# Performance work log

Measured on AMD Instinct MI355X. Metric: run time of the kernel, lower is better.

## Reference

```python
import jax, jax.numpy as jnp
import numpy as np

EPS = 1e-12  # F.normalize denominator clamp


def setup_inputs() -> dict:
    key = jax.random.key(0)
    k1, k2, k3, k4 = jax.random.split(key, 4)
    bs, d, nc, ncl, cs, ny = 8192, 768, 64, 500, 100, 1000
    train_embedding = jax.random.normal(k1, (bs, d), dtype=jnp.float32)
    clusters = jax.random.normal(k2, (ncl, cs, d), dtype=jnp.float32)
    # init_concept: uniform in [-0.5, 0.5]
    concept = jax.random.uniform(k3, (d, nc), dtype=jnp.float32, minval=-0.5, maxval=0.5)
    W_h = jax.random.normal(k4, (d, ny), dtype=jnp.float32) * 0.02
    b_h = jnp.zeros((ny,), dtype=jnp.float32)
    return {"train_embedding": train_embedding, "clusters": clusters,
            "concept": concept, "W_h": W_h, "b_h": b_h}


def reference(train_embedding, clusters, concept, W_h, b_h):
    # column-wise L2 normalize concept (F.normalize p=2 dim=0)
    concept_normalized = concept / jnp.maximum(
        jnp.linalg.norm(concept, axis=0, keepdims=True), EPS)
    # projection onto span(concept): C (C^T C)^-1 C^T
    gram = concept.T @ concept                      # [nc, nc]
    proj_matrix = concept @ jnp.linalg.inv(gram) @ concept.T  # [d, d]
    proj = proj_matrix @ train_embedding.T          # [d, bs]
    cluster_mean = jnp.mean(clusters, axis=1)       # [ncl, d]
    score_matrix = jnp.abs(cluster_mean @ concept_normalized)  # [ncl, nc]
    score_norm = score_matrix / jnp.maximum(
        jnp.linalg.norm(score_matrix, axis=0, keepdims=True), EPS)
    L_sparse_1 = jnp.sum(score_norm)
    # sum_{i != j} <score_norm[:,i], score_norm[:,j]> == sum(G) - trace(G)
    G = score_norm.T @ score_norm                   # [nc, nc]
    L_sparse_2 = jnp.sum(G) - jnp.trace(G)
    y_pred = proj.T @ W_h + b_h                     # h_x as linear head, [bs, ny]
    return (y_pred, L_sparse_1, L_sparse_2)
```

## Files before the change

kernel.cpp:

```cpp
#include <hip/hip_runtime.h>
#include <hip/hip_bf16.h>
#include <math.h>

#define BS   8192
#define DD   768
#define NC   64
#define NCL  500
#define CS   100
#define NY   1000
#define EPSN 1e-12f

typedef __attribute__((ext_vector_type(8))) short bf16x8;
typedef __attribute__((ext_vector_type(4))) float f32x4;

union B8 { unsigned u[4]; bf16x8 v; uint4 q; };

__device__ inline unsigned short f2bf(float x) {
    __hip_bfloat16 h = __float2bfloat16(x);
    return *reinterpret_cast<unsigned short*>(&h);
}
__device__ inline unsigned pk2(float a, float b) {
    return (unsigned)f2bf(a) | ((unsigned)f2bf(b) << 16);
}

#define FMA4(acc, s, v) { (acc).x = fmaf((s), (v).x, (acc).x); \
                          (acc).y = fmaf((s), (v).y, (acc).y); \
                          (acc).z = fmaf((s), (v).z, (acc).z); \
                          (acc).w = fmaf((s), (v).w, (acc).w); }

__global__ __launch_bounds__(256) void k_front(
    const float* __restrict__ clusters, const float* __restrict__ C,
    const float* __restrict__ W, const float* __restrict__ X,
    float* __restrict__ cmP, float* __restrict__ gramP,
    float* __restrict__ Up, unsigned short* __restrict__ Tb) {
    __shared__ __align__(16) char smem_raw[25600];
    int b = blockIdx.x, tid = threadIdx.x;
    if (b < 128) {
        uint4 (*CbL)[64] = (uint4(*)[64])smem_raw;
        int r0 = b * 64;
        int w  = tid >> 6, l = tid & 63;
        int rowA = r0 + w*16 + (l & 15);
        int kq   = l >> 4;
        const float* xb = X + (size_t)rowA * DD + kq * 8;
        f32x4 acc[4];
        #pragma unroll
        for (int ng = 0; ng < 4; ++ng) acc[ng] = (f32x4){0.f, 0.f, 0.f, 0.f};
        for (int kc = 0; kc < DD; kc += 64) {
            __syncthreads();
            #pragma unroll
            for (int u = 0; u < 2; ++u) {
                int g = (tid >> 6) + u*4;
                int n = tid & 63;
                const float* cp = C + (size_t)(kc + g*8) * 64 + n;
                uint4 gr;
                gr.x = pk2(cp[0],   cp[64]);
                gr.y = pk2(cp[128], cp[192]);
                gr.z = pk2(cp[256], cp[320]);
                gr.w = pk2(cp[384], cp[448]);
                CbL[g][n] = gr;
            }
            __syncthreads();
            #pragma unroll
            for (int ks2 = 0; ks2 < 2; ++ks2) {
                float4 xa = *((const float4*)(xb + kc + ks2*32));
                float4 xc = *((const float4*)(xb + kc + ks2*32 + 4));
                B8 a;
                a.u[0] = pk2(xa.x, xa.y); a.u[1] = pk2(xa.z, xa.w);
                a.u[2] = pk2(xc.x, xc.y); a.u[3] = pk2(xc.z, xc.w);
                B8 b0, b1, b2, b3;
                b0.q = CbL[ks2*4 + kq][(l & 15)];
                b1.q = CbL[ks2*4 + kq][(l & 15) + 16];
                b2.q = CbL[ks2*4 + kq][(l & 15) + 32];
                b3.q = CbL[ks2*4 + kq][(l & 15) + 48];
                acc[0] = __builtin_amdgcn_mfma_f32_16x16x32_bf16(a.v, b0.v, acc[0], 0, 0, 0);
                acc[1] = __builtin_amdgcn_mfma_f32_16x16x32_bf16(a.v, b1.v, acc[1], 0, 0, 0);
                acc[2] = __builtin_amdgcn_mfma_f32_16x16x32_bf16(a.v, b2.v, acc[2], 0, 0, 0);
                acc[3] = __builtin_amdgcn_mfma_f32_16x16x32_bf16(a.v, b3.v, acc[3], 0, 0, 0);
            }
        }
        int rw = r0 + w*16 + kq * 4;
        #pragma unroll
        for (int ng = 0; ng < 4; ++ng) {
            int n = ng*16 + (l & 15);
            #pragma unroll
            for (int r = 0; r < 4; ++r)
                Tb[(size_t)(rw + r) * 64 + n] = f2bf(acc[ng][r]);
        }
    } else if (b < 1628) {
        int q   = b - 128;
        int sp  = q & 3;
        int idx = (q >> 2) * 256 + tid;
        int r  = idx / 192;
        int d4 = idx % 192;
        const float4* base = (const float4*)clusters
                           + (size_t)r * CS * 192 + (size_t)sp * 25 * 192 + d4;
        float4 a0={0,0,0,0},a1={0,0,0,0},a2={0,0,0,0},a3={0,0,0,0},a4={0,0,0,0};
        for (int s = 0; s < 25; s += 5) {
            float4 v0 = base[(size_t)(s+0)*192];
            float4 v1 = base[(size_t)(s+1)*192];
            float4 v2 = base[(size_t)(s+2)*192];
            float4 v3 = base[(size_t)(s+3)*192];
            float4 v4 = base[(size_t)(s+4)*192];
            a0.x+=v0.x; a0.y+=v0.y; a0.z+=v0.z; a0.w+=v0.w;
            a1.x+=v1.x; a1.y+=v1.y; a1.z+=v1.z; a1.w+=v1.w;
            a2.x+=v2.x; a2.y+=v2.y; a2.z+=v2.z; a2.w+=v2.w;
            a3.x+=v3.x; a3.y+=v3.y; a3.z+=v3.z; a3.w+=v3.w;
            a4.x+=v4.x; a4.y+=v4.y; a4.z+=v4.z; a4.w+=v4.w;
        }
        float4 o;
        o.x = a0.x+a1.x+a2.x+a3.x+a4.x;
        o.y = a0.y+a1.y+a2.y+a3.y+a4.y;
        o.z = a0.z+a1.z+a2.z+a3.z+a4.z;
        o.w = a0.w+a1.w+a2.w+a3.w+a4.w;
        ((float4*)(cmP + (size_t)sp * 384000))[idx] = o;
    } else if (b < 1884) {
        int q  = b - 1628;
        int j  = q & 63, ks = q >> 6;
        int i   = tid & 63;
        int seg = tid >> 6;
        int k0  = ks * 192 + seg * 48;
        float p = 0.f;
        for (int k = k0; k < k0 + 48; ++k)
            p += C[k * NC + i] * C[k * NC + j];
        float (*red)[64] = (float(*)[64])smem_raw;
        red[seg][i] = p;
        __syncthreads();
        if (seg == 0)
            gramP[(size_t)ks * 4096 + i * NC + j] =
                red[0][i] + red[1][i] + red[2][i] + red[3][i];
    } else {
        int q  = b - 1884;
        int nt = q >> 2, ks = q & 3;
        int n0 = nt * 128, kb = ks * 192;
        float (*Cu)[68]  = (float(*)[68])smem_raw;
        float (*Wu)[132] = (float(*)[132])(smem_raw + 8704);
        int tx = tid & 15, ty = tid >> 4;
        float4 a0[4], a1[4];
        #pragma unroll
        for (int i = 0; i < 4; ++i) { a0[i] = make_float4(0,0,0,0); a1[i] = make_float4(0,0,0,0); }
        for (int kc = kb; kc < kb + 192; kc += 32) {
            __syncthreads();
            {   int i4 = tid & 15, kk = tid >> 4;
                *((float4*)&Cu[kk][i4*4])    = *((const float4*)(C + (size_t)(kc+kk)*64 + i4*4));
                *((float4*)&Cu[kk+16][i4*4]) = *((const float4*)(C + (size_t)(kc+kk+16)*64 + i4*4));
            }
            {   int nf = tid & 31, kq2 = tid >> 5;
                #pragma unroll
                for (int u = 0; u < 4; ++u) {
                    int k = kq2 + u * 8;
                    int n = n0 + nf * 4;
                    float4 v = {0.f, 0.f, 0.f, 0.f};
                    if (n < NY) v = *((const float4*)(W + (size_t)(kc + k) * NY + n));
                    *((float4*)&Wu[k][nf*4]) = v;
                }
            }
            __syncthreads();
            #pragma unroll 8
            for (int k = 0; k < 32; ++k) {
                float4 ci = *((float4*)&Cu[k][ty*4]);
                float4 w0 = *((float4*)&Wu[k][tx*8]);
                float4 w1 = *((float4*)&Wu[k][tx*8+4]);
                FMA4(a0[0], ci.x, w0); FMA4(a1[0], ci.x, w1);
                FMA4(a0[1], ci.y, w0); FMA4(a1[1], ci.y, w1);
                FMA4(a0[2], ci.z, w0); FMA4(a1[2], ci.z, w1);
                FMA4(a0[3], ci.w, w0); FMA4(a1[3], ci.w, w1);
            }
        }
        float* Ups = Up + (size_t)ks * 64000;
        #pragma unroll
        for (int i = 0; i < 4; ++i) {
            int irow = ty * 4 + i;
            int n = n0 + tx * 8;
            if (n < NY)     *((float4*)(Ups + (size_t)irow * NY + n))     = a0[i];
            if (n + 4 < NY) *((float4*)(Ups + (size_t)irow * NY + n + 4)) = a1[i];
        }
    }
}

__global__ __launch_bounds__(256) void k_mid(
    const float* __restrict__ gramP, const float* __restrict__ cmP,
    const float* __restrict__ C, float* __restrict__ ginv,
    float* __restrict__ SP) {
    __shared__ __align__(16) char smem_raw[52224];
    int blk = blockIdx.x, tid = threadIdx.x;
    if (blk == 0) {
        int c = tid & 63;
        int q = tid >> 6;
        float a[16], bb[16];
        #pragma unroll
        for (int i = 0; i < 16; ++i) {
            int r = q * 16 + i;
            size_t off = (size_t)r * 64 + c;
            a[i]  = gramP[off] + gramP[4096 + off] + gramP[8192 + off] + gramP[12288 + off];
            bb[i] = (r == c) ? 1.f : 0.f;
        }
        __shared__ float asr[2][64];
        __shared__ float bsr[2][64];
        for (int p = 0; p < 64; ++p) {
            int qp  = p >> 4;
            int lp  = p & 15;
            int par = p & 1;
            if (q == qp) {
                float ap = 0.f, bp = 0.f;
                #pragma unroll
                for (int i = 0; i < 16; ++i)
                    if (i == lp) { ap = a[i]; bp = bb[i]; }
                float App = __shfl(ap, p);
                float s   = 1.0f / App;
                asr[par][c] = ap * s;
                bsr[par][c] = bp * s;
            }
            __syncthreads();
            float as_ = asr[par][c];
            float bs_ = bsr[par][c];
            #pragma unroll
            for (int i = 0; i < 16; ++i) {
                float f = __shfl(a[i], p);
                bool isp = (q == qp) && (i == lp);
                a[i]  = isp ? as_ : fmaf(-f, as_, a[i]);
                bb[i] = isp ? bs_ : fmaf(-f, bs_, bb[i]);
            }
        }
        #pragma unroll
        for (int i = 0; i < 16; ++i)
            ginv[(q * 16 + i) * 64 + c] = bb[i];
    } else {
        int q = blk - 1;
        int tile = q >> 2, ks = q & 3;
        int r0 = tile * 128, kb = ks * 192;
        float (*Mr)[68] = (float(*)[68])smem_raw;
        float (*Cs)[68] = (float(*)[68])(smem_raw + 128*68*4);
        int tx = tid & 15, ty = tid >> 4;
        float4 acc[8];
        #pragma unroll
        for (int r = 0; r < 8; ++r) acc[r] = make_float4(0.f,0.f,0.f,0.f);
        for (int kc = 0; kc < 192; kc += 64) {
            __syncthreads();
            #pragma unroll
            for (int p = 0; p < 8; ++p) {
                int f = tid + p * 256;
                int row = f >> 4, k4 = f & 15;
                int gr = r0 + row;
                int grc = gr < NCL ? gr : (NCL - 1);
                size_t off = (size_t)grc*DD + kb + kc + k4*4;
                float4 c0 = *((const float4*)(cmP + off));
                float4 c1 = *((const float4*)(cmP + 384000 + off));
                float4 c2 = *((const float4*)(cmP + 768000 + off));
                float4 c3 = *((const float4*)(cmP + 1152000 + off));
                float4 m;
                m.x = (c0.x+c1.x+c2.x+c3.x) * 0.01f;
                m.y = (c0.y+c1.y+c2.y+c3.y) * 0.01f;
                m.z = (c0.z+c1.z+c2.z+c3.z) * 0.01f;
                m.w = (c0.w+c1.w+c2.w+c3.w) * 0.01f;
                *((float4*)&Mr[row][k4*4]) = m;
            }
            #pragma unroll
            for (int p = 0; p < 4; ++p) {
                int f = tid + p * 256;
                int k = f >> 4, c4 = f & 15;
                *((float4*)&Cs[k][c4*4]) =
                    *((const float4*)(C + (size_t)(kb+kc+k)*64 + c4*4));
            }
            __syncthreads();
            for (int k0 = 0; k0 < 64; k0 += 4) {
                float4 cv0 = *((float4*)&Cs[k0+0][tx*4]);
                float4 cv1 = *((float4*)&Cs[k0+1][tx*4]);
                float4 cv2 = *((float4*)&Cs[k0+2][tx*4]);
                float4 cv3 = *((float4*)&Cs[k0+3][tx*4]);
                #pragma unroll
                for (int r = 0; r < 8; ++r) {
                    float4 xv = *((float4*)&Mr[ty*8+r][k0]);
                    FMA4(acc[r], xv.x, cv0);
                    FMA4(acc[r], xv.y, cv1);
                    FMA4(acc[r], xv.z, cv2);
                    FMA4(acc[r], xv.w, cv3);
                }
            }
        }
        float* SPs = SP + (size_t)ks * 32000;
        #pragma unroll
        for (int r = 0; r < 8; ++r) {
            int row = r0 + ty * 8 + r;
            if (row < NCL)
                *((float4*)(SPs + (size_t)row * 64 + tx*4)) = acc[r];
        }
    }
}

__global__ __launch_bounds__(256) void k_vc(
    const float* __restrict__ ginv, const float* __restrict__ Up,
    float* __restrict__ SP, unsigned short* __restrict__ Vb,
    float* __restrict__ out2) {
    __shared__ __align__(16) char smem_raw[34816];
    int blk = blockIdx.x, tid = threadIdx.x;
    if (blk == 16) {
        __shared__ float colred[4][64];
        __shared__ float rn[64];
        __shared__ float trc[64];
        __shared__ float r1[4], r2[4];
        const float* SP0 = SP;
        const float* SP1 = SP + 32000;
        const float* SP2 = SP + 64000;
        const float* SP3 = SP + 96000;
        int c = tid & 63, seg = tid >> 6;
        float p = 0.f;
        for (int r = seg; r < NCL; r += 4) {
            int off = r * 64 + c;
            float s = fabsf(SP0[off] + SP1[off] + SP2[off] + SP3[off]);
            SP[off] = s;
            p += s * s;
        }
        colred[seg][c] = p;
        __syncthreads();
        if (seg == 0) {
            float n2  = colred[0][c] + colred[1][c] + colred[2][c] + colred[3][c];
            float inv = 1.0f / fmaxf(sqrtf(n2), EPSN);
            rn[c]  = inv;
            trc[c] = n2 * inv * inv;
        }
        __syncthreads();
        float l1p = 0.f, l2p = 0.f;
        for (int r = tid; r < NCL; r += 256) {
            float rs = 0.f;
            #pragma unroll
            for (int cc = 0; cc < 64; ++cc)
                rs += SP[r * 64 + cc] * rn[cc];
            l1p += rs;
            l2p += rs * rs;
        }
        #pragma unroll
        for (int off = 32; off > 0; off >>= 1) {
            l1p += __shfl_down(l1p, off);
            l2p += __shfl_down(l2p, off);
        }
        int wave = tid >> 6, lane = tid & 63;
        if (lane == 0) { r1[wave] = l1p; r2[wave] = l2p; }
        __syncthreads();
        if (tid == 0) {
            float L1 = r1[0] + r1[1] + r1[2] + r1[3];
            float L2 = r2[0] + r2[1] + r2[2] + r2[3];
            float tr = 0.f;
            #pragma unroll
            for (int cc = 0; cc < 64; ++cc) tr += trc[cc];
            out2[0] = L1;
            out2[1] = L2 - tr;
        }
        return;
    }
    float (*Us)[68] = (float(*)[68])smem_raw;
    float (*Gs)[68] = (float(*)[68])(smem_raw + 64*68*4);
    int c0 = blk * 64;
    int tx = tid & 15, ty = tid >> 4;
    const float* Up0 = Up;
    const float* Up1 = Up + 64000;
    const float* Up2 = Up + 128000;
    const float* Up3 = Up + 192000;
    #pragma unroll
    for (int p = 0; p < 4; ++p) {
        int f = tid + p * 256;
        int j = f >> 4, n4 = f & 15;
        int n = c0 + n4 * 4;
        float4 v = {0.f, 0.f, 0.f, 0.f};
        if (n < NY) {
            float4 u0 = *((const float4*)(Up0 + (size_t)j * NY + n));
            float4 u1 = *((const float4*)(Up1 + (size_t)j * NY + n));
            float4 u2 = *((const float4*)(Up2 + (size_t)j * NY + n));
            float4 u3 = *((const float4*)(Up3 + (size_t)j * NY + n));
            v.x = u0.x + u1.x + u2.x + u3.x;
            v.y = u0.y + u1.y + u2.y + u3.y;
            v.z = u0.z + u1.z + u2.z + u3.z;
            v.w = u0.w + u1.w + u2.w + u3.w;
        }
        *((float4*)&Us[j][n4*4]) = v;
        *((float4*)&Gs[j][n4*4]) = *((const float4*)(ginv + (size_t)j * 64 + n4*4));
    }
    __syncthreads();
    float4 acc[4];
    #pragma unroll
    for (int i = 0; i < 4; ++i) acc[i] = make_float4(0.f,0.f,0.f,0.f);
    for (int j0 = 0; j0 < 64; j0 += 4) {
        #pragma unroll
        for (int jj = 0; jj < 4; ++jj) {
            float4 g = *((float4*)&Gs[j0+jj][ty*4]);
            float4 u = *((float4*)&Us[j0+jj][tx*4]);
            FMA4(acc[0], g.x, u);
            FMA4(acc[1], g.y, u);
            FMA4(acc[2], g.z, u);
            FMA4(acc[3], g.w, u);
        }
    }
    #pragma unroll
    for (int i = 0; i < 4; ++i) {
        int krow = ty * 4 + i;
        Vb[(size_t)(c0 + tx*4 + 0) * 64 + krow] = f2bf(acc[i].x);
        Vb[(size_t)(c0 + tx*4 + 1) * 64 + krow] = f2bf(acc[i].y);
        Vb[(size_t)(c0 + tx*4 + 2) * 64 + krow] = f2bf(acc[i].z);
        Vb[(size_t)(c0 + tx*4 + 3) * 64 + krow] = f2bf(acc[i].w);
    }
}

__global__ __launch_bounds__(256) void k_ypred(
    const uint4* __restrict__ Tb, const uint4* __restrict__ Vbq,
    const float* __restrict__ bh, float* __restrict__ Y) {
    int blk = blockIdx.x, tid = threadIdx.x;
    int rb = blk >> 3, cb = blk & 7;
    int r0g = rb * 128, c0g = cb * 128;
    int w = tid >> 6, l = tid & 63;
    int wr = (w >> 1) * 64, wc = (w & 1) * 64;
    int kq = l >> 4, ln = l & 15;
    f32x4 acc[4][4];
    #pragma unroll
    for (int rg = 0; rg < 4; ++rg)
        #pragma unroll
        for (int ng = 0; ng < 4; ++ng) acc[rg][ng] = (f32x4){0.f,0.f,0.f,0.f};
    #pragma unroll
    for (int ks = 0; ks < 2; ++ks) {
        B8 a[4], bb[4];
        #pragma unroll
        for (int rg = 0; rg < 4; ++rg) {
            int row = r0g + wr + rg*16 + ln;
            a[rg].q = Tb[(size_t)row * 8 + ks*4 + kq];
        }
        #pragma unroll
        for (int ng = 0; ng < 4; ++ng) {
            int n = c0g + wc + ng*16 + ln;
            bb[ng].q = Vbq[(size_t)n * 8 + ks*4 + kq];
        }
        #pragma unroll
        for (int rg = 0; rg < 4; ++rg)
            #pragma unroll
            for (int ng = 0; ng < 4; ++ng)
                acc[rg][ng] = __builtin_amdgcn_mfma_f32_16x16x32_bf16(
                    a[rg].v, bb[ng].v, acc[rg][ng], 0, 0, 0);
    }
    #pragma unroll
    for (int ng = 0; ng < 4; ++ng) {
        int n = c0g + wc + ng*16 + ln;
        if (n < NY) {
            float bias = bh[n];
            #pragma unroll
            for (int rg = 0; rg < 4; ++rg) {
                int row = r0g + wr + rg*16 + kq*4;
                #pragma unroll
                for (int r = 0; r < 4; ++r)
                    Y[(size_t)(row + r) * NY + n] = acc[rg][ng][r] + bias;
            }
        }
    }
}

extern "C" void kernel_launch(void* const* d_in, const int* in_sizes, int n_in,
                              void* d_out, int out_size, void* d_ws, size_t ws_size,
                              hipStream_t stream) {
    const float* X        = (const float*)d_in[0];
    const float* clusters = (const float*)d_in[1];
    const float* C        = (const float*)d_in[2];
    const float* W        = (const float*)d_in[3];
    const float* bh       = (const float*)d_in[4];
    float* out = (float*)d_out;
    float* ws  = (float*)d_ws;

    float* cmP   = ws;
    float* gramP = cmP   + 1536000;
    float* ginv  = gramP + 16384;
    float* Up    = ginv  + 4096;
    float* SP    = Up    + 256000;
    float* TbF   = SP    + 128000;
    float* VbF   = TbF   + 262144;

    unsigned short* Tb  = (unsigned short*)TbF;
    unsigned short* Vb  = (unsigned short*)VbF;

    k_front <<<dim3(1916), dim3(256), 0, stream>>>(clusters, C, W, X, cmP, gramP, Up, Tb);
    k_mid   <<<dim3(17),   dim3(256), 0, stream>>>(gramP, cmP, C, ginv, SP);
    k_vc    <<<dim3(17),   dim3(256), 0, stream>>>(ginv, Up, SP, Vb, out + (size_t)BS * NY);
    k_ypred <<<dim3(512),  dim3(256), 0, stream>>>((const uint4*)Tb, (const uint4*)Vb, bh, out);
}
```

Before: 161.0 us.

## Fold cluster mean into MFMA projection of raw clusters onto concepts

Instead of reducing the clusters tensor to its per-cluster means and then multiplying by the concept matrix, each cluster sample is projected directly onto the concept matrix with bf16 MFMA in k_front (200 blocks, 25 sample splits). The partial products are then summed and abs'd in a small k_mid reduction. This drops the cmP workspace and the fp32 FMA score GEMM in k_mid. In exchange it does about 100x more matrix FLOPs on the large clusters tensor and rounds the inputs to bf16. The per-sample scale of 1/100 is also dropped, which column normalization cancels but which changes the unnormalized score path.

```diff
diff --git a/kernel.cpp b/kernel.cpp
--- a/kernel.cpp
+++ b/kernel.cpp
@@ -31,13 +31,71 @@
 __global__ __launch_bounds__(256) void k_front(
     const float* __restrict__ clusters, const float* __restrict__ C,
     const float* __restrict__ W, const float* __restrict__ X,
-    float* __restrict__ cmP, float* __restrict__ gramP,
-    float* __restrict__ Up, unsigned short* __restrict__ Tb) {
+    float* __restrict__ gramP, float* __restrict__ Up,
+    float* __restrict__ SP, unsigned short* __restrict__ Tb) {
     __shared__ __align__(16) char smem_raw[25600];
     int b = blockIdx.x, tid = threadIdx.x;
-    if (b < 128) {
+    if (b < 200) {
+        int rt = b / 25, sp = b % 25;
         uint4 (*CbL)[64] = (uint4(*)[64])smem_raw;
-        int r0 = b * 64;
+        int r0 = rt * 64;
+        int w  = tid >> 6, l = tid & 63;
+        int rowA = r0 + w*16 + (l & 15);
+        int rcl  = rowA < NCL ? rowA : (NCL - 1);
+        int kq   = l >> 4;
+        const float* ab = clusters + (size_t)rcl * CS * DD + (size_t)sp * 4 * DD + kq * 8;
+        f32x4 acc[4];
+        #pragma unroll
+        for (int ng = 0; ng < 4; ++ng) acc[ng] = (f32x4){0.f, 0.f, 0.f, 0.f};
+        for (int kc = 0; kc < DD; kc += 64) {
+            __syncthreads();
+            #pragma unroll
+            for (int u = 0; u < 2; ++u) {
+                int g = (tid >> 6) + u*4;
+                int n = tid & 63;
+                const float* cp = C + (size_t)(kc + g*8) * 64 + n;
+                uint4 gr;
+                gr.x = pk2(cp[0],   cp[64]);
+                gr.y = pk2(cp[128], cp[192]);
+                gr.z = pk2(cp[256], cp[320]);
+                gr.w = pk2(cp[384], cp[448]);
+                CbL[g][n] = gr;
+            }
+            __syncthreads();
+            #pragma unroll
+            for (int ss = 0; ss < 4; ++ss) {
+                #pragma unroll
+                for (int ks2 = 0; ks2 < 2; ++ks2) {
+                    const float* ap = ab + (size_t)ss * DD + kc + ks2*32;
+                    float4 xa = *((const float4*)ap);
+                    float4 xc = *((const float4*)(ap + 4));
+                    B8 a;
+                    a.u[0] = pk2(xa.x, xa.y); a.u[1] = pk2(xa.z, xa.w);
+                    a.u[2] = pk2(xc.x, xc.y); a.u[3] = pk2(xc.z, xc.w);
+                    B8 b0, b1, b2, b3;
+                    b0.q = CbL[ks2*4 + kq][(l & 15)];
+                    b1.q = CbL[ks2*4 + kq][(l & 15) + 16];
+                    b2.q = CbL[ks2*4 + kq][(l & 15) + 32];
+                    b3.q = CbL[ks2*4 + kq][(l & 15) + 48];
+                    acc[0] = __builtin_amdgcn_mfma_f32_16x16x32_bf16(a.v, b0.v, acc[0], 0, 0, 0);
+                    acc[1] = __builtin_amdgcn_mfma_f32_16x16x32_bf16(a.v, b1.v, acc[1], 0, 0, 0);
+                    acc[2] = __builtin_amdgcn_mfma_f32_16x16x32_bf16(a.v, b2.v, acc[2], 0, 0, 0);
+                    acc[3] = __builtin_amdgcn_mfma_f32_16x16x32_bf16(a.v, b3.v, acc[3], 0, 0, 0);
+                }
+            }
+        }
+        int rw = r0 + w*16 + kq * 4;
+        float* SPs = SP + (size_t)sp * 32768;
+        #pragma unroll
+        for (int ng = 0; ng < 4; ++ng) {
+            int n = ng*16 + (l & 15);
+            #pragma unroll
+            for (int r = 0; r < 4; ++r)
+                SPs[(size_t)(rw + r) * 64 + n] = acc[ng][r];
+        }
+    } else if (b < 328) {
+        uint4 (*CbL)[64] = (uint4(*)[64])smem_raw;
+        int r0 = (b - 200) * 64;
         int w  = tid >> 6, l = tid & 63;
         int rowA = r0 + w*16 + (l & 15);
         int kq   = l >> 4;
@@ -86,35 +144,8 @@
             for (int r = 0; r < 4; ++r)
                 Tb[(size_t)(rw + r) * 64 + n] = f2bf(acc[ng][r]);
         }
-    } else if (b < 1628) {
-        int q   = b - 128;
-        int sp  = q & 3;
-        int idx = (q >> 2) * 256 + tid;
-        int r  = idx / 192;
-        int d4 = idx % 192;
-        const float4* base = (const float4*)clusters
-                           + (size_t)r * CS * 192 + (size_t)sp * 25 * 192 + d4;
-        float4 a0={0,0,0,0},a1={0,0,0,0},a2={0,0,0,0},a3={0,0,0,0},a4={0,0,0,0};
-        for (int s = 0; s < 25; s += 5) {
-            float4 v0 = base[(size_t)(s+0)*192];
-            float4 v1 = base[(size_t)(s+1)*192];
-            float4 v2 = base[(size_t)(s+2)*192];
-            float4 v3 = base[(size_t)(s+3)*192];
-            float4 v4 = base[(size_t)(s+4)*192];
-            a0.x+=v0.x; a0.y+=v0.y; a0.z+=v0.z; a0.w+=v0.w;
-            a1.x+=v1.x; a1.y+=v1.y; a1.z+=v1.z; a1.w+=v1.w;
-            a2.x+=v2.x; a2.y+=v2.y; a2.z+=v2.z; a2.w+=v2.w;
-            a3.x+=v3.x; a3.y+=v3.y; a3.z+=v3.z; a3.w+=v3.w;
-            a4.x+=v4.x; a4.y+=v4.y; a4.z+=v4.z; a4.w+=v4.w;
-        }
-        float4 o;
-        o.x = a0.x+a1.x+a2.x+a3.x+a4.x;
-        o.y = a0.y+a1.y+a2.y+a3.y+a4.y;
-        o.z = a0.z+a1.z+a2.z+a3.z+a4.z;
-        o.w = a0.w+a1.w+a2.w+a3.w+a4.w;
-        ((float4*)(cmP + (size_t)sp * 384000))[idx] = o;
-    } else if (b < 1884) {
-        int q  = b - 1628;
+    } else if (b < 584) {
+        int q  = b - 328;
         int j  = q & 63, ks = q >> 6;
         int i   = tid & 63;
         int seg = tid >> 6;
@@ -129,7 +160,7 @@
             gramP[(size_t)ks * 4096 + i * NC + j] =
                 red[0][i] + red[1][i] + red[2][i] + red[3][i];
     } else {
-        int q  = b - 1884;
+        int q  = b - 584;
         int nt = q >> 2, ks = q & 3;
         int n0 = nt * 128, kb = ks * 192;
         float (*Cu)[68]  = (float(*)[68])smem_raw;
@@ -178,10 +209,8 @@
 }
 
 __global__ __launch_bounds__(256) void k_mid(
-    const float* __restrict__ gramP, const float* __restrict__ cmP,
-    const float* __restrict__ C, float* __restrict__ ginv,
-    float* __restrict__ SP) {
-    __shared__ __align__(16) char smem_raw[52224];
+    const float* __restrict__ gramP, const float* __restrict__ SP,
+    float* __restrict__ ginv, float* __restrict__ Sfin) {
     int blk = blockIdx.x, tid = threadIdx.x;
     if (blk == 0) {
         int c = tid & 63;
@@ -225,71 +254,24 @@
         for (int i = 0; i < 16; ++i)
             ginv[(q * 16 + i) * 64 + c] = bb[i];
     } else {
-        int q = blk - 1;
-        int tile = q >> 2, ks = q & 3;
-        int r0 = tile * 128, kb = ks * 192;
-        float (*Mr)[68] = (float(*)[68])smem_raw;
-        float (*Cs)[68] = (float(*)[68])(smem_raw + 128*68*4);
-        int tx = tid & 15, ty = tid >> 4;
-        float4 acc[8];
-        #pragma unroll
-        for (int r = 0; r < 8; ++r) acc[r] = make_float4(0.f,0.f,0.f,0.f);
-        for (int kc = 0; kc < 192; kc += 64) {
-            __syncthreads();
-            #pragma unroll
-            for (int p = 0; p < 8; ++p) {
-                int f = tid + p * 256;
-                int row = f >> 4, k4 = f & 15;
-                int gr = r0 + row;
-                int grc = gr < NCL ? gr : (NCL - 1);
-                size_t off = (size_t)grc*DD + kb + kc + k4*4;
-                float4 c0 = *((const float4*)(cmP + off));
-                float4 c1 = *((const float4*)(cmP + 384000 + off));
-                float4 c2 = *((const float4*)(cmP + 768000 + off));
-                float4 c3 = *((const float4*)(cmP + 1152000 + off));
-                float4 m;
-                m.x = (c0.x+c1.x+c2.x+c3.x) * 0.01f;
-                m.y = (c0.y+c1.y+c2.y+c3.y) * 0.01f;
-                m.z = (c0.z+c1.z+c2.z+c3.z) * 0.01f;
-                m.w = (c0.w+c1.w+c2.w+c3.w) * 0.01f;
-                *((float4*)&Mr[row][k4*4]) = m;
-            }
-            #pragma unroll
-            for (int p = 0; p < 4; ++p) {
-                int f = tid + p * 256;
-                int k = f >> 4, c4 = f & 15;
-                *((float4*)&Cs[k][c4*4]) =
-                    *((const float4*)(C + (size_t)(kb+kc+k)*64 + c4*4));
-            }
-            __syncthreads();
-            for (int k0 = 0; k0 < 64; k0 += 4) {
-                float4 cv0 = *((float4*)&Cs[k0+0][tx*4]);
-                float4 cv1 = *((float4*)&Cs[k0+1][tx*4]);
-                float4 cv2 = *((float4*)&Cs[k0+2][tx*4]);
-                float4 cv3 = *((float4*)&Cs[k0+3][tx*4]);
-                #pragma unroll
-                for (int r = 0; r < 8; ++r) {
-                    float4 xv = *((float4*)&Mr[ty*8+r][k0]);
-                    FMA4(acc[r], xv.x, cv0);
-                    FMA4(acc[r], xv.y, cv1);
-                    FMA4(acc[r], xv.z, cv2);
-                    FMA4(acc[r], xv.w, cv3);
-                }
-            }
-        }
-        float* SPs = SP + (size_t)ks * 32000;
-        #pragma unroll
-        for (int r = 0; r < 8; ++r) {
-            int row = r0 + ty * 8 + r;
-            if (row < NCL)
-                *((float4*)(SPs + (size_t)row * 64 + tx*4)) = acc[r];
+        int e = blk - 1;
+        for (int t = tid; t < 1000; t += 256) {
+            size_t off = (size_t)e * 4000 + (size_t)t * 4;
+            float4 s = {0.f, 0.f, 0.f, 0.f};
+            #pragma unroll
+            for (int p = 0; p < 25; ++p) {
+                float4 v = *((const float4*)(SP + (size_t)p * 32768 + off));
+                s.x += v.x; s.y += v.y; s.z += v.z; s.w += v.w;
+            }
+            float4 o = {fabsf(s.x), fabsf(s.y), fabsf(s.z), fabsf(s.w)};
+            *((float4*)(Sfin + off)) = o;
         }
     }
 }
 
 __global__ __launch_bounds__(256) void k_vc(
     const float* __restrict__ ginv, const float* __restrict__ Up,
-    float* __restrict__ SP, unsigned short* __restrict__ Vb,
+    const float* __restrict__ Sfin, unsigned short* __restrict__ Vb,
     float* __restrict__ out2) {
     __shared__ __align__(16) char smem_raw[34816];
     int blk = blockIdx.x, tid = threadIdx.x;
@@ -298,16 +280,10 @@
         __shared__ float rn[64];
         __shared__ float trc[64];
         __shared__ float r1[4], r2[4];
-        const float* SP0 = SP;
-        const float* SP1 = SP + 32000;
-        const float* SP2 = SP + 64000;
-        const float* SP3 = SP + 96000;
         int c = tid & 63, seg = tid >> 6;
         float p = 0.f;
         for (int r = seg; r < NCL; r += 4) {
-            int off = r * 64 + c;
-            float s = fabsf(SP0[off] + SP1[off] + SP2[off] + SP3[off]);
-            SP[off] = s;
+            float s = Sfin[r * 64 + c];
             p += s * s;
         }
         colred[seg][c] = p;
@@ -324,7 +300,7 @@
             float rs = 0.f;
             #pragma unroll
             for (int cc = 0; cc < 64; ++cc)
-                rs += SP[r * 64 + cc] * rn[cc];
+                rs += Sfin[r * 64 + cc] * rn[cc];
             l1p += rs;
             l2p += rs * rs;
         }
@@ -460,19 +436,19 @@
     float* out = (float*)d_out;
     float* ws  = (float*)d_ws;
 
-    float* cmP   = ws;
-    float* gramP = cmP   + 1536000;
+    float* gramP = ws;
     float* ginv  = gramP + 16384;
     float* Up    = ginv  + 4096;
     float* SP    = Up    + 256000;
-    float* TbF   = SP    + 128000;
+    float* Sfin  = SP    + 819200;
+    float* TbF   = Sfin  + 32768;
     float* VbF   = TbF   + 262144;
 
     unsigned short* Tb  = (unsigned short*)TbF;
     unsigned short* Vb  = (unsigned short*)VbF;
 
-    k_front <<<dim3(1916), dim3(256), 0, stream>>>(clusters, C, W, X, cmP, gramP, Up, Tb);
-    k_mid   <<<dim3(17),   dim3(256), 0, stream>>>(gramP, cmP, C, ginv, SP);
-    k_vc    <<<dim3(17),   dim3(256), 0, stream>>>(ginv, Up, SP, Vb, out + (size_t)BS * NY);
-    k_ypred <<<dim3(512),  dim3(256), 0, stream>>>((const uint4*)Tb, (const uint4*)Vb, bh, out);
-}
+    k_front <<<dim3(616), dim3(256), 0, stream>>>(clusters, C, W, X, gramP, Up, SP, Tb);
+    k_mid   <<<dim3(9),   dim3(256), 0, stream>>>(gramP, SP, ginv, Sfin);
+    k_vc    <<<dim3(17),  dim3(256), 0, stream>>>(ginv, Up, Sfin, Vb, out + (size_t)BS * NY);
+    k_ypred <<<dim3(512), dim3(256), 0, stream>>>((const uint4*)Tb, (const uint4*)Vb, bh, out);
+}
```

Result: faster. 146.6 us (-9.0%).
